# Kernel optimization log

Measured on AMD Instinct MI355X. Metric: run time of the kernel, lower is better.

Reference implementation:

```python
import jax, jax.numpy as jnp
import numpy as np

B, L, H, E = 8, 4096, 8, 64  # in_channels = out_channels = H*E = 512
MODES = 64                   # mode_select_method='else' -> indices = range(MODES)
SCALE = 1.0 / (512 * 512)


def setup_inputs() -> dict:
    key = jax.random.key(0)
    kq, kk, kv, k1, k2 = jax.random.split(key, 5)
    q = jax.random.normal(kq, (B, L, H, E), dtype=jnp.float32)
    k = jax.random.normal(kk, (B, L, H, E), dtype=jnp.float32)
    v = jax.random.normal(kv, (B, L, H, E), dtype=jnp.float32)
    # weights: [num_heads, in_ch//heads, out_ch//heads, modes], scaled randn
    w1 = SCALE * jax.random.normal(k1, (H, E, E, MODES), dtype=jnp.float32)
    w2 = SCALE * jax.random.normal(k2, (H, E, E, MODES), dtype=jnp.float32)
    return {"q": q, "k": k, "v": v, "w1": w1, "w2": w2}


def reference(q, k, v, w1, w2):
    # k, v, mask are unused by FourierBlock.forward
    Bq, Lq, Hq, Eq = q.shape
    modes = w1.shape[-1]
    x = jnp.transpose(q, (0, 2, 3, 1))          # [B, H, E, L]
    x_ft = jnp.fft.rfft(x, axis=-1)             # [B, H, E, L//2+1] complex
    # With mode_select_method='else', selected indices are 0..modes-1.
    W = (w1 + 1j * w2).astype(x_ft.dtype)       # [H, E_in, E_out, modes]
    # Fused gather + batched complex matmul over all modes (replaces the per-mode loop)
    out_ft = jnp.einsum('bhim,hiom->bhom', x_ft[..., :modes], W)  # [B, H, E, modes]
    # irfft with n=L zero-pads the freq axis from `modes` up to L//2+1 (FEDformer quirk)
    x_out = jnp.fft.irfft(out_ft, n=Lq, axis=-1)  # [B, H, E, L] real
    return jnp.transpose(x_out, (0, 3, 1, 2))     # [B, L, H, E]
```

## Files before the change

kernel.cpp:

```cpp
#include <hip/hip_runtime.h>
#include <hip/hip_bf16.h>
#include <math.h>

#define NB 8
#define LN 4096
#define NH 8
#define NE 64
#define NC 512
#define NM 64
#define LMASK 4095

typedef short s16x8 __attribute__((ext_vector_type(8)));
typedef float f32x4 __attribute__((ext_vector_type(4)));
typedef const __attribute__((address_space(1))) void gv_t;
typedef __attribute__((address_space(3))) void lv_t;

#define WS_TF  262144
#define WS_GF  524288
#define WS_XP  786432
#define WS_XS  4980736

static __device__ __forceinline__ unsigned short bf16bits(float f) {
    __hip_bfloat16 b = __float2bfloat16(f);
    return *reinterpret_cast<unsigned short*>(&b);
}

__global__ __launch_bounds__(256, 3) void k_fs1(const float* __restrict__ q,
                                                float* __restrict__ xp) {
    __shared__ float qlds[4][4][32][16];
    __shared__ unsigned short eglds[2][4096];
    const int ks = blockIdx.x, h = blockIdx.y, b = blockIdx.z;
    const int tid = threadIdx.x;
    const int w = tid >> 6, lane = tid & 63;
    const int g = lane >> 4, r = lane & 15;

    const float* qsrc = q + (((size_t)b * LN + ks * 512 + (lane >> 2)) * NH + h) * NE
                          + w * 16 + (lane & 3) * 4;

    const int m_tw  = (tid >> 5) * 8 + (tid & 7);
    const int kg_tw = (tid >> 3) & 3;

#define STAGE_Q(T) { \
    __builtin_amdgcn_global_load_lds((gv_t*)(qsrc + (size_t)(T) * 32 * NC), \
        (lv_t*)(&qlds[(T) & 3][w][0][0]), 16, 0, 0); \
    __builtin_amdgcn_global_load_lds((gv_t*)(qsrc + ((size_t)(T) * 32 + 16) * NC), \
        (lv_t*)(&qlds[(T) & 3][w][16][0]), 16, 0, 0); }

    f32x4 acc[8];
    #pragma unroll
    for (int mt = 0; mt < 8; ++mt) acc[mt] = (f32x4)(0.0f);

    STAGE_Q(0) STAGE_Q(1) STAGE_Q(2)

    #pragma unroll
    for (int t = 0; t < 16; ++t) {
        {
            const int kc = ks * 16 + t;
            int tw = (m_tw * (kc * 32 + kg_tw * 8)) & LMASK;
            unsigned short vc[8], vs[8];
            #pragma unroll
            for (int j = 0; j < 8; ++j) {
                float ang = (6.283185307179586f / 4096.0f) * (float)tw;
                vc[j] = bf16bits(__cosf(ang));
                vs[j] = bf16bits(-__sinf(ang));
                tw = (tw + m_tw) & LMASK;
            }
            uint4 p0, p1;
            p0.x = (unsigned)vc[0] | ((unsigned)vc[1] << 16);
            p0.y = (unsigned)vc[2] | ((unsigned)vc[3] << 16);
            p0.z = (unsigned)vc[4] | ((unsigned)vc[5] << 16);
            p0.w = (unsigned)vc[6] | ((unsigned)vc[7] << 16);
            p1.x = (unsigned)vs[0] | ((unsigned)vs[1] << 16);
            p1.y = (unsigned)vs[2] | ((unsigned)vs[3] << 16);
            p1.z = (unsigned)vs[4] | ((unsigned)vs[5] << 16);
            p1.w = (unsigned)vs[6] | ((unsigned)vs[7] << 16);
            *reinterpret_cast<uint4*>(&eglds[t & 1][tid * 16])     = p0;
            *reinterpret_cast<uint4*>(&eglds[t & 1][tid * 16 + 8]) = p1;
        }
        if (t <= 13)      asm volatile("s_waitcnt vmcnt(4)" ::: "memory");
        else if (t == 14) asm volatile("s_waitcnt vmcnt(2)" ::: "memory");
        else              asm volatile("s_waitcnt vmcnt(0)" ::: "memory");
        asm volatile("s_waitcnt lgkmcnt(0)" ::: "memory");
        __builtin_amdgcn_s_barrier();
        asm volatile("" ::: "memory");
        if (t + 3 < 16) STAGE_Q(t + 3)

        s16x8 af[8];
        #pragma unroll
        for (int mt = 0; mt < 8; ++mt)
            af[mt] = *reinterpret_cast<const s16x8*>(&eglds[t & 1][mt * 512 + lane * 8]);
        s16x8 bfr;
        #pragma unroll
        for (int j = 0; j < 8; ++j)
            bfr[j] = (short)bf16bits(qlds[t & 3][w][g * 8 + j][r]);

        __builtin_amdgcn_s_setprio(1);
        #pragma unroll
        for (int mt = 0; mt < 8; ++mt)
            acc[mt] = __builtin_amdgcn_mfma_f32_16x16x32_bf16(af[mt], bfr, acc[mt], 0, 0, 0);
        __builtin_amdgcn_s_setprio(0);
    }
#undef STAGE_Q

    const int i = w * 16 + r;
    float* xpb = xp + ((size_t)ks * 64 + b * 8 + h) * (64 * 128) + (size_t)i * 128 + g * 4;
    #pragma unroll
    for (int mt = 0; mt < 8; ++mt)
        *reinterpret_cast<f32x4*>(xpb + mt * 16) = acc[mt];
}

__global__ __launch_bounds__(256) void k_presum(const float* __restrict__ xp,
                                                float* __restrict__ xs,
                                                unsigned short* __restrict__ tfp) {
    const int bid = blockIdx.x;
    if (bid < 512) {
        int e4 = bid * 256 + threadIdx.x;
        const f32x4* xp4 = reinterpret_cast<const f32x4*>(xp);
        f32x4 s = (f32x4)(0.0f);
        #pragma unroll
        for (int ks = 0; ks < 8; ++ks)
            s += __builtin_nontemporal_load(&xp4[(size_t)ks * 131072 + e4]);
        reinterpret_cast<f32x4*>(xs)[e4] = s;
        return;
    }
    const int s = (bid - 512) * 256 + threadIdx.x;
    const int lane = s & 63;
    const int lt = (s >> 6) & 255, kk = s >> 14;
    const int l = lt * 16 + (lane & 15);
    const int khi = (lane >> 4) * 8;
    unsigned short v[8];
    #pragma unroll
    for (int j = 0; j < 8; ++j) {
        int mp = kk * 32 + khi + j;
        int m = mp >> 1;
        int tw = (m * l) & LMASK;
        float ang = (6.283185307179586f / 4096.0f) * (float)tw;
        v[j] = bf16bits((mp & 1) ? sinf(ang) : cosf(ang));
    }
    uint4 pk;
    pk.x = (unsigned)v[0] | ((unsigned)v[1] << 16);
    pk.y = (unsigned)v[2] | ((unsigned)v[3] << 16);
    pk.z = (unsigned)v[4] | ((unsigned)v[5] << 16);
    pk.w = (unsigned)v[6] | ((unsigned)v[7] << 16);
    *reinterpret_cast<uint4*>(tfp + (size_t)s * 8) = pk;
}

__global__ __launch_bounds__(256) void k_s2(const float* __restrict__ w1,
                                            const float* __restrict__ w2,
                                            const float* __restrict__ xs,
                                            unsigned short* __restrict__ gf) {
    __shared__ float2 sxs[2][64][64];
    const int sid = blockIdx.x;
    const int x   = sid & 7;
    const int idx = sid >> 3;
    const int r   = x * 8 + (idx & 7);
    const int og  = r >> 3, h = r & 7;
    const int bb  = idx >> 3;
    const int tt  = threadIdx.x;

    {
        float4* dst = reinterpret_cast<float4*>(&sxs[0][0][0]);
        #pragma unroll
        for (int bs = 0; bs < 2; ++bs) {
            const float4* s4 = reinterpret_cast<const float4*>(
                xs + ((size_t)((bb * 2 + bs) * 8 + h)) * 8192);
            #pragma unroll
            for (int k = 0; k < 8; ++k)
                dst[bs * 2048 + k * 256 + tt] = s4[k * 256 + tt];
        }
    }
    __syncthreads();

    const int m    = tt & 63;
    const int osub = tt >> 6;
    const int o0   = og * 8 + osub * 2;

    float re[2][2], im[2][2];
    #pragma unroll
    for (int oo = 0; oo < 2; ++oo)
        #pragma unroll
        for (int bs = 0; bs < 2; ++bs) { re[oo][bs] = 0.f; im[oo][bs] = 0.f; }

    const float* w1p = w1 + (size_t)h * (NE * NE * NM) + (size_t)o0 * NM + m;
    const float* w2p = w2 + (size_t)h * (NE * NE * NM) + (size_t)o0 * NM + m;

    #pragma unroll 8
    for (int i = 0; i < NE; ++i) {
        float wr0 = w1p[(size_t)i * (NE * NM)];
        float wi0 = w2p[(size_t)i * (NE * NM)];
        float wr1 = w1p[(size_t)i * (NE * NM) + NM];
        float wi1 = w2p[(size_t)i * (NE * NM) + NM];
        #pragma unroll
        for (int bs = 0; bs < 2; ++bs) {
            float2 xv = sxs[bs][i][m];
            re[0][bs] = fmaf(xv.x, wr0, fmaf(-xv.y, wi0, re[0][bs]));
            im[0][bs] = fmaf(xv.x, wi0, fmaf( xv.y, wr0, im[0][bs]));
            re[1][bs] = fmaf(xv.x, wr1, fmaf(-xv.y, wi1, re[1][bs]));
            im[1][bs] = fmaf(xv.x, wi1, fmaf( xv.y, wr1, im[1][bs]));
        }
    }

    const float sca = (m == 0 ? 1.0f : 2.0f) / (float)LN;
    const int kk  = m >> 4;
    const int khi = ((m & 15) >> 2) * 16;
    const int jj  = (m & 3) << 1;
    #pragma unroll
    for (int oo = 0; oo < 2; ++oo) {
        const int c = h * 64 + o0 + oo;
        #pragma unroll
        for (int bs = 0; bs < 2; ++bs) {
            const int b = bb * 2 + bs;
            size_t slot = (((size_t)b * 4 + kk) * 32 + (c >> 4)) * 64 + khi + (c & 15);
            unsigned int pk = (unsigned)bf16bits(re[oo][bs] * sca) |
                              ((unsigned)bf16bits(-im[oo][bs] * sca) << 16);
            *reinterpret_cast<unsigned int*>(gf + slot * 8 + jj) = pk;
        }
    }
}

__global__ __launch_bounds__(256, 2) void k_s3(const unsigned short* __restrict__ gf,
                                               const unsigned short* __restrict__ tfp,
                                               float* __restrict__ out) {
    const int lb = blockIdx.x;
    const int cb = blockIdx.y;
    const int b  = blockIdx.z;
    const int tid = threadIdx.x;
    const int w = tid >> 6, lane = tid & 63;

    const unsigned short* ga = gf + ((((size_t)b * 4) * 32 + cb * 8 + w * 2) * 64 + lane) * 8;
    const unsigned short* tb = tfp + (((size_t)lb * 4) * 64 + lane) * 8;

    f32x4 acc[2][4] = {};
    s16x8 af[3][2], bf[3][4];

#define S3_LOAD(T, SLOT)                                                          \
    {                                                                             \
        const unsigned short* gp_ = ga + (size_t)(T) * (32 * 64 * 8);             \
        const unsigned short* tp_ = tb + (size_t)(T) * (256 * 64 * 8);            \
        af[SLOT][0] = *reinterpret_cast<const s16x8*>(gp_);                       \
        af[SLOT][1] = *reinterpret_cast<const s16x8*>(gp_ + 64 * 8);              \
        bf[SLOT][0] = *reinterpret_cast<const s16x8*>(tp_);                       \
        bf[SLOT][1] = *reinterpret_cast<const s16x8*>(tp_ + 64 * 8);              \
        bf[SLOT][2] = *reinterpret_cast<const s16x8*>(tp_ + 2 * 64 * 8);          \
        bf[SLOT][3] = *reinterpret_cast<const s16x8*>(tp_ + 3 * 64 * 8);          \
    }

    S3_LOAD(0, 0)
    S3_LOAD(1, 1)

    #pragma unroll
    for (int t = 0; t < 4; ++t) {
        const int slot = t % 3;
        if (t + 2 < 4) { const int ns = (t + 2) % 3; S3_LOAD(t + 2, ns) }
        __builtin_amdgcn_s_setprio(1);
        #pragma unroll
        for (int mi = 0; mi < 2; ++mi)
            #pragma unroll
            for (int ni = 0; ni < 4; ++ni)
                acc[mi][ni] = __builtin_amdgcn_mfma_f32_16x16x32_bf16(
                    af[slot][mi], bf[slot][ni], acc[mi][ni], 0, 0, 0);
        __builtin_amdgcn_s_setprio(0);
    }
#undef S3_LOAD

    const int c0 = cb * 128 + w * 32 + (lane >> 4) * 4;
    const int l0 = lb * 64 + (lane & 15);
    #pragma unroll
    for (int mi = 0; mi < 2; ++mi)
        #pragma unroll
        for (int ni = 0; ni < 4; ++ni) {
            float* op = out + ((size_t)b * LN + l0 + ni * 16) * NC + c0 + mi * 16;
            __builtin_nontemporal_store(acc[mi][ni], reinterpret_cast<f32x4*>(op));
        }
}

extern "C" void kernel_launch(void* const* d_in, const int* in_sizes, int n_in,
                              void* d_out, int out_size, void* d_ws, size_t ws_size,
                              hipStream_t stream) {
    const float* q  = (const float*)d_in[0];
    const float* w1 = (const float*)d_in[3];
    const float* w2 = (const float*)d_in[4];
    float* out = (float*)d_out;
    float* ws  = (float*)d_ws;

    unsigned short* tfp = (unsigned short*)(ws + WS_TF);
    unsigned short* gf  = (unsigned short*)(ws + WS_GF);
    float*          xp  = ws + WS_XP;
    float*          xs  = ws + WS_XS;

    k_fs1<<<dim3(8, NH, NB), 256, 0, stream>>>(q, xp);
    k_presum<<<768, 256, 0, stream>>>(xp, xs, tfp);
    k_s2<<<256, 256, 0, stream>>>(w1, w2, xs, gf);
    k_s3<<<dim3(64, 4, NB), 256, 0, stream>>>(gf, tfp, out);
}
```

Measured before the change: 50.77 us.

## Fuse partial-sum reduction and twiddle generation into the spectral mixing kernel

Removes the separate presum kernel. Each mixing block now sums the eight split-L partial spectra directly while staging into LDS, and extra blocks in the same launch generate the twiddle table. This drops one kernel launch and the intermediate xs buffer round-trip. In exchange, each (batch, head) partial slice is re-read and re-summed by every output-group block, which multiplies the global/L2 read traffic.

Result: no change. 50.23 us (-1.1%).

```diff
diff --git a/kernel.cpp b/kernel.cpp
--- a/kernel.cpp
+++ b/kernel.cpp
@@ -18,7 +18,6 @@
 #define WS_TF  262144
 #define WS_GF  524288
 #define WS_XP  786432
-#define WS_XS  4980736
 
 static __device__ __forceinline__ unsigned short bf16bits(float f) {
     __hip_bfloat16 b = __float2bfloat16(f);
@@ -109,64 +108,57 @@
         *reinterpret_cast<f32x4*>(xpb + mt * 16) = acc[mt];
 }
 
-__global__ __launch_bounds__(256) void k_presum(const float* __restrict__ xp,
-                                                float* __restrict__ xs,
-                                                unsigned short* __restrict__ tfp) {
-    const int bid = blockIdx.x;
-    if (bid < 512) {
-        int e4 = bid * 256 + threadIdx.x;
-        const f32x4* xp4 = reinterpret_cast<const f32x4*>(xp);
-        f32x4 s = (f32x4)(0.0f);
-        #pragma unroll
-        for (int ks = 0; ks < 8; ++ks)
-            s += __builtin_nontemporal_load(&xp4[(size_t)ks * 131072 + e4]);
-        reinterpret_cast<f32x4*>(xs)[e4] = s;
-        return;
-    }
-    const int s = (bid - 512) * 256 + threadIdx.x;
-    const int lane = s & 63;
-    const int lt = (s >> 6) & 255, kk = s >> 14;
-    const int l = lt * 16 + (lane & 15);
-    const int khi = (lane >> 4) * 8;
-    unsigned short v[8];
-    #pragma unroll
-    for (int j = 0; j < 8; ++j) {
-        int mp = kk * 32 + khi + j;
-        int m = mp >> 1;
-        int tw = (m * l) & LMASK;
-        float ang = (6.283185307179586f / 4096.0f) * (float)tw;
-        v[j] = bf16bits((mp & 1) ? sinf(ang) : cosf(ang));
-    }
-    uint4 pk;
-    pk.x = (unsigned)v[0] | ((unsigned)v[1] << 16);
-    pk.y = (unsigned)v[2] | ((unsigned)v[3] << 16);
-    pk.z = (unsigned)v[4] | ((unsigned)v[5] << 16);
-    pk.w = (unsigned)v[6] | ((unsigned)v[7] << 16);
-    *reinterpret_cast<uint4*>(tfp + (size_t)s * 8) = pk;
-}
-
 __global__ __launch_bounds__(256) void k_s2(const float* __restrict__ w1,
                                             const float* __restrict__ w2,
-                                            const float* __restrict__ xs,
-                                            unsigned short* __restrict__ gf) {
+                                            const float* __restrict__ xp,
+                                            unsigned short* __restrict__ gf,
+                                            unsigned short* __restrict__ tfp) {
     __shared__ float2 sxs[2][64][64];
-    const int sid = blockIdx.x;
-    const int x   = sid & 7;
-    const int idx = sid >> 3;
-    const int r   = x * 8 + (idx & 7);
-    const int og  = r >> 3, h = r & 7;
-    const int bb  = idx >> 3;
-    const int tt  = threadIdx.x;
+    const int bid = blockIdx.x;
+    if (bid >= 256) {
+        const int s = (bid - 256) * 256 + threadIdx.x;
+        const int lane = s & 63;
+        const int lt = (s >> 6) & 255, kk = s >> 14;
+        const int l = lt * 16 + (lane & 15);
+        const int khi = (lane >> 4) * 8;
+        unsigned short v[8];
+        #pragma unroll
+        for (int j = 0; j < 8; ++j) {
+            int mp = kk * 32 + khi + j;
+            int m = mp >> 1;
+            int tw = (m * l) & LMASK;
+            float ang = (6.283185307179586f / 4096.0f) * (float)tw;
+            v[j] = bf16bits((mp & 1) ? sinf(ang) : cosf(ang));
+        }
+        uint4 pk;
+        pk.x = (unsigned)v[0] | ((unsigned)v[1] << 16);
+        pk.y = (unsigned)v[2] | ((unsigned)v[3] << 16);
+        pk.z = (unsigned)v[4] | ((unsigned)v[5] << 16);
+        pk.w = (unsigned)v[6] | ((unsigned)v[7] << 16);
+        *reinterpret_cast<uint4*>(tfp + (size_t)s * 8) = pk;
+        return;
+    }
+
+    const int og = bid >> 5;
+    const int bb = (bid >> 3) & 3;
+    const int h  = bid & 7;
+    const int tt = threadIdx.x;
 
     {
-        float4* dst = reinterpret_cast<float4*>(&sxs[0][0][0]);
+        f32x4* dst = reinterpret_cast<f32x4*>(&sxs[0][0][0]);
+        const f32x4* xp4 = reinterpret_cast<const f32x4*>(xp);
         #pragma unroll
         for (int bs = 0; bs < 2; ++bs) {
-            const float4* s4 = reinterpret_cast<const float4*>(
-                xs + ((size_t)((bb * 2 + bs) * 8 + h)) * 8192);
+            const size_t base = (size_t)((bb * 2 + bs) * 8 + h) * 2048;
             #pragma unroll
-            for (int k = 0; k < 8; ++k)
-                dst[bs * 2048 + k * 256 + tt] = s4[k * 256 + tt];
+            for (int k = 0; k < 8; ++k) {
+                f32x4 s = (f32x4)(0.0f);
+                #pragma unroll
+                for (int ks = 0; ks < 8; ++ks)
+                    s += __builtin_nontemporal_load(
+                        &xp4[(size_t)ks * 131072 + base + k * 256 + tt]);
+                dst[bs * 2048 + k * 256 + tt] = s;
+            }
         }
     }
     __syncthreads();
@@ -286,10 +278,8 @@
     unsigned short* tfp = (unsigned short*)(ws + WS_TF);
     unsigned short* gf  = (unsigned short*)(ws + WS_GF);
     float*          xp  = ws + WS_XP;
-    float*          xs  = ws + WS_XS;
 
     k_fs1<<<dim3(8, NH, NB), 256, 0, stream>>>(q, xp);
-    k_presum<<<768, 256, 0, stream>>>(xp, xs, tfp);
-    k_s2<<<256, 256, 0, stream>>>(w1, w2, xs, gf);
+    k_s2<<<512, 256, 0, stream>>>(w1, w2, xp, gf, tfp);
     k_s3<<<dim3(64, 4, NB), 256, 0, stream>>>(gf, tfp, out);
 }
```
